# Performance work log

Hardware: AMD Instinct MI355X
Metric: run time of the kernel (lower is better)

The kernel has to match this reference:

```python
import jax, jax.numpy as jnp
import numpy as np

BLOCK = 64


def setup_inputs() -> dict:
    key = jax.random.key(0)
    ks = jax.random.split(key, 8)
    B, S, H = 16, 2048, 768
    E, M, P = 32, 4, 128
    L = 97
    return {
        "task_features": jax.random.normal(ks[0], (B, S, H), dtype=jnp.float32),
        "entity_position_ids": jax.random.randint(ks[1], (B, E, M), 0, S),
        "head_tail_idxs": jax.random.randint(ks[2], (B, P, 2), 0, E),
        "Wh": jax.random.normal(ks[3], (H, H), dtype=jnp.float32) * 0.02,
        "bh": jnp.zeros((H,), dtype=jnp.float32),
        "Wt": jax.random.normal(ks[4], (H, H), dtype=jnp.float32) * 0.02,
        "bt": jnp.zeros((H,), dtype=jnp.float32),
        "Wc": jax.random.normal(ks[5], (H * BLOCK, L), dtype=jnp.float32) * 0.02,
        "bc": jnp.zeros((L,), dtype=jnp.float32),
    }


def reference(task_features, entity_position_ids, head_tail_idxs, Wh, bh, Wt, bt, Wc, bc):
    B, S, H = task_features.shape
    pos = entity_position_ids  # [B, E, M] mention start positions
    # One-hot semantics: indicator[start]=1, so duplicate mention positions within an
    # entity count once. Keep only first occurrence of each position per entity.
    eq = pos[..., :, None] == pos[..., None, :]          # [B, E, M, M]
    dup = jnp.any(jnp.tril(eq, -1), axis=-1)             # equal to an earlier mention
    w = (~dup).astype(task_features.dtype)               # [B, E, M]
    # Gather mention-start features and pool (sum) per entity: [B, E, H]
    feats = task_features[jnp.arange(B)[:, None, None], pos]  # [B, E, M, H]
    ent = jnp.einsum('bemh,bem->beh', feats, w)
    # Select subject/object entity representations per pair
    bi = jnp.arange(B)[:, None]
    subj = ent[bi, head_tail_idxs[..., 0]].reshape(-1, H)  # [B*P, H]
    obj = ent[bi, head_tail_idxs[..., 1]].reshape(-1, H)
    z_s = jnp.tanh(subj @ Wh + bh)
    z_o = jnp.tanh(obj @ Wt + bt)
    N = z_s.shape[0]
    b1 = z_s.reshape(N, H // BLOCK, BLOCK)
    b2 = z_o.reshape(N, H // BLOCK, BLOCK)
    # Block-bilinear: per-block outer product -> [N, H*BLOCK]
    bl = (b1[..., :, None] * b2[..., None, :]).reshape(N, H * BLOCK)
    logits = bl @ Wc + bc  # [N, 97]
    return logits
```

## Files before the change

kernel.cpp:

```cpp
#include <hip/hip_runtime.h>
#include <hip/hip_bf16.h>

typedef __bf16 bf16_t;
typedef bf16_t bf16x8 __attribute__((ext_vector_type(8)));
typedef float  f32x4  __attribute__((ext_vector_type(4)));

#define B_    16
#define S_    2048
#define H_    768
#define E_    32
#define M_    4
#define P_    128
#define L_    97
#define NPAIR 2048
#define RSPLIT 48

#define OFF_WHT  0u
#define OFF_WTT  (OFF_WHT + 768u*768u*2u)
#define OFF_WCG  (OFF_WTT + 768u*768u*2u)
#define OFF_ENT  (OFF_WCG + 768u*14336u)
#define OFF_ZS   (OFF_ENT + 512u*768u*2u)
#define OFF_ZO   (OFF_ZS  + 512u*768u*2u)
#define OFF_PART (OFF_ZO  + 512u*768u*2u)

typedef __attribute__((address_space(1))) const unsigned gu32;
typedef __attribute__((address_space(3))) unsigned lu32;

static __device__ __forceinline__ float bf_lo(unsigned u) { return __builtin_bit_cast(float, u << 16); }
static __device__ __forceinline__ float bf_hi(unsigned u) { return __builtin_bit_cast(float, u & 0xffff0000u); }
static __device__ __forceinline__ unsigned short bf_bits(float f) {
    return __builtin_bit_cast(unsigned short, (bf16_t)f);
}

__global__ __launch_bounds__(256) void k_transpose_w(const float* __restrict__ Wh,
                                                     const float* __restrict__ Wt,
                                                     bf16_t* __restrict__ whT,
                                                     bf16_t* __restrict__ wtT) {
    __shared__ float tile[32][33];
    const float* W = blockIdx.z ? Wt : Wh;
    bf16_t* WT = blockIdx.z ? wtT : whT;
    int k0 = blockIdx.x * 32, c0 = blockIdx.y * 32;
    int tx = threadIdx.x & 31, ty = threadIdx.x >> 5;
    for (int r = 0; r < 4; r++) {
        int ky = ty + r * 8;
        tile[ky][tx] = W[(k0 + ky) * H_ + c0 + tx];
    }
    __syncthreads();
    for (int r = 0; r < 4; r++) {
        int cy = ty + r * 8;
        WT[(c0 + cy) * H_ + (k0 + tx)] = (bf16_t)tile[tx][cy];
    }
}

__global__ __launch_bounds__(256) void k_build_wcg(const float* __restrict__ Wc,
                                                   unsigned* __restrict__ wcg) {
    int I = blockIdx.x;
    unsigned base_dw = (unsigned)I * 3584u;
    for (int r = 0; r < 14; r++) {
        int d  = threadIdx.x + 256 * r;
        int l  = d >> 5;
        int gp = (d >> 2) & 7;
        int k  = d & 3;
        int gl = gp ^ (l & 7);
        int j  = (gl * 4 + k) * 2;
        int p  = I * 64 + j;
        float v0 = (l < L_) ? Wc[(size_t)p * L_ + l]       : 0.f;
        float v1 = (l < L_) ? Wc[(size_t)(p + 1) * L_ + l] : 0.f;
        unsigned pk = (unsigned)bf_bits(v0) | ((unsigned)bf_bits(v1) << 16);
        wcg[base_dw + d] = pk;
    }
}

__global__ __launch_bounds__(256) void k_ent(const float* __restrict__ tf,
                                             const int* __restrict__ pos,
                                             bf16_t* __restrict__ ent) {
    int be = blockIdx.x;
    int b  = be >> 5;
    int p0 = pos[be*4+0], p1 = pos[be*4+1], p2 = pos[be*4+2], p3 = pos[be*4+3];
    bool w1 = (p1 != p0);
    bool w2 = (p2 != p0) && (p2 != p1);
    bool w3 = (p3 != p0) && (p3 != p1) && (p3 != p2);
    const float* base = tf + (size_t)b * S_ * H_;
    for (int qq = 0; qq < 3; qq++) {
        int h = threadIdx.x + qq * 256;
        float s = base[(size_t)p0 * H_ + h];
        if (w1) s += base[(size_t)p1 * H_ + h];
        if (w2) s += base[(size_t)p2 * H_ + h];
        if (w3) s += base[(size_t)p3 * H_ + h];
        ent[(size_t)be * H_ + h] = (bf16_t)s;
    }
}

__global__ __launch_bounds__(256) void k_gemm_z(const bf16_t* __restrict__ ent,
                                                const bf16_t* __restrict__ whT,
                                                const bf16_t* __restrict__ wtT,
                                                const float* __restrict__ bh,
                                                const float* __restrict__ bt,
                                                bf16_t* __restrict__ zs,
                                                bf16_t* __restrict__ zo) {
    const bf16_t* WT  = blockIdx.z ? wtT : whT;
    const float* bias = blockIdx.z ? bt  : bh;
    bf16_t* outp      = blockIdx.z ? zo  : zs;
    int w = threadIdx.x >> 6, lane = threadIdx.x & 63;
    int ml = lane & 15, q = lane >> 4;
    int m0 = blockIdx.x * 64 + w * 16;
    int c0 = blockIdx.y * 64;
    f32x4 zero4 = {0.f, 0.f, 0.f, 0.f};
    f32x4 acc[4] = {zero4, zero4, zero4, zero4};
    const bf16_t* aptr = ent + (size_t)(m0 + ml) * H_ + q * 8;
    for (int kk = 0; kk < 24; kk++) {
        bf16x8 a = *reinterpret_cast<const bf16x8*>(aptr + kk * 32);
        for (int lt = 0; lt < 4; lt++) {
            const bf16_t* bp = WT + (size_t)(c0 + lt * 16 + ml) * H_ + kk * 32 + q * 8;
            bf16x8 bfr = *reinterpret_cast<const bf16x8*>(bp);
            acc[lt] = __builtin_amdgcn_mfma_f32_16x16x32_bf16(a, bfr, acc[lt], 0, 0, 0);
        }
    }
    for (int lt = 0; lt < 4; lt++)
        for (int r = 0; r < 4; r++) {
            int row = q * 4 + r;
            int col = c0 + lt * 16 + ml;
            float v = tanhf(acc[lt][r] + bias[col]);
            outp[(size_t)(m0 + row) * H_ + col] = (bf16_t)v;
        }
}

__global__ __launch_bounds__(256) void k_bilinear(const bf16_t* __restrict__ zs,
                                                  const bf16_t* __restrict__ zo,
                                                  const unsigned* __restrict__ wcg,
                                                  const int* __restrict__ ht,
                                                  float* __restrict__ pout) {
    __shared__ __align__(16) unsigned wc_lds[2][112 * 32];
    __shared__ unsigned short zs_lds[16 * 256];
    int nb = blockIdx.x;
    int c  = blockIdx.y;
    int I0 = c * 16;
    int kblk = I0 >> 6;
    int i0   = I0 & 63;
    int t = threadIdx.x;
    int w = t >> 6, lane = t & 63, ml = lane & 15, q = lane >> 4;
    int nbase = nb * 256;

    {
        int n  = nbase + t;
        int es = (n >> 7) * E_ + ht[n * 2 + 0];
        const unsigned short* src =
            reinterpret_cast<const unsigned short*>(zs) + (size_t)es * H_ + kblk * 64 + i0;
        uint4 u0 = *reinterpret_cast<const uint4*>(src);
        uint4 u1 = *reinterpret_cast<const uint4*>(src + 8);
        unsigned vals[8] = {u0.x, u0.y, u0.z, u0.w, u1.x, u1.y, u1.z, u1.w};
        for (int d = 0; d < 8; d++) {
            zs_lds[(2 * d) * 256 + t]     = (unsigned short)(vals[d] & 0xffffu);
            zs_lds[(2 * d + 1) * 256 + t] = (unsigned short)(vals[d] >> 16);
        }
    }

    bf16x8 zoA[4][2];
    for (int nt = 0; nt < 4; nt++) {
        int n  = nbase + w * 64 + nt * 16 + ml;
        int eo = (n >> 7) * E_ + ht[n * 2 + 1];
        const bf16_t* src = zo + (size_t)eo * H_ + kblk * 64;
        zoA[nt][0] = *reinterpret_cast<const bf16x8*>(src + 0 * 32 + q * 8);
        zoA[nt][1] = *reinterpret_cast<const bf16x8*>(src + 1 * 32 + q * 8);
    }

    f32x4 zero4 = {0.f, 0.f, 0.f, 0.f};
    f32x4 acc[4][7];
    for (int nt = 0; nt < 4; nt++)
        for (int lt = 0; lt < 7; lt++) acc[nt][lt] = zero4;

    const unsigned* gsrc = wcg + (size_t)I0 * 3584u;

    for (int pp = w; pp < 14; pp += 4)
        __builtin_amdgcn_global_load_lds((gu32*)(gsrc + pp * 256 + lane * 4),
                                         (lu32*)&wc_lds[0][pp * 256], 16, 0, 0);
    __syncthreads();

    int sw = ml & 7;
    for (int ii = 0; ii < 16; ii++) {
        int pb = ii & 1;
        if (ii < 15) {
            const unsigned* g2 = gsrc + (size_t)(ii + 1) * 3584u;
            for (int pp = w; pp < 14; pp += 4)
                __builtin_amdgcn_global_load_lds((gu32*)(g2 + pp * 256 + lane * 4),
                                                 (lu32*)&wc_lds[1 - pb][pp * 256], 16, 0, 0);
        }

        float zsv[4][4];
        for (int nt = 0; nt < 4; nt++) {
            const unsigned* zp = reinterpret_cast<const unsigned*>(
                &zs_lds[ii * 256 + w * 64 + nt * 16 + q * 4]);
            unsigned z0 = zp[0], z1 = zp[1];
            zsv[nt][0] = bf_lo(z0); zsv[nt][1] = bf_hi(z0);
            zsv[nt][2] = bf_lo(z1); zsv[nt][3] = bf_hi(z1);
        }

        const unsigned short* wch = reinterpret_cast<const unsigned short*>(wc_lds[pb]);
        for (int lt = 0; lt < 7; lt++) {
            int l = lt * 16 + ml;
            bf16x8 b0 = *reinterpret_cast<const bf16x8*>(wch + l * 64 + ((q ^ sw) * 8));
            bf16x8 b1 = *reinterpret_cast<const bf16x8*>(wch + l * 64 + (((4 + q) ^ sw) * 8));
            for (int nt = 0; nt < 4; nt++) {
                f32x4 dres = __builtin_amdgcn_mfma_f32_16x16x32_bf16(zoA[nt][0], b0, zero4, 0, 0, 0);
                dres = __builtin_amdgcn_mfma_f32_16x16x32_bf16(zoA[nt][1], b1, dres, 0, 0, 0);
                for (int r = 0; r < 4; r++) acc[nt][lt][r] += zsv[nt][r] * dres[r];
            }
        }
        __syncthreads();
    }

    float* po = pout + ((size_t)c * NPAIR + nbase) * 112;
    for (int nt = 0; nt < 4; nt++)
        for (int lt = 0; lt < 7; lt++)
            for (int r = 0; r < 4; r++) {
                int nl = w * 64 + nt * 16 + q * 4 + r;
                po[(size_t)nl * 112 + lt * 16 + ml] = acc[nt][lt][r];
            }
}

__global__ __launch_bounds__(256) void k_reduce(const float* __restrict__ part,
                                                const float* __restrict__ bc,
                                                float* __restrict__ out) {
    int t = blockIdx.x * 256 + threadIdx.x;
    if (t >= NPAIR * L_) return;
    int n = t / L_;
    int l = t - n * L_;
    float s = bc[l];
    const float* p = part + (size_t)n * 112 + l;
    #pragma unroll
    for (int cc = 0; cc < RSPLIT; cc++) s += p[(size_t)cc * NPAIR * 112];
    out[t] = s;
}

extern "C" void kernel_launch(void* const* d_in, const int* in_sizes, int n_in,
                              void* d_out, int out_size, void* d_ws, size_t ws_size,
                              hipStream_t stream) {
    (void)in_sizes; (void)n_in; (void)out_size; (void)ws_size;
    const float* tf  = (const float*)d_in[0];
    const int*   pos = (const int*)d_in[1];
    const int*   ht  = (const int*)d_in[2];
    const float* Wh  = (const float*)d_in[3];
    const float* bh  = (const float*)d_in[4];
    const float* Wt  = (const float*)d_in[5];
    const float* bt  = (const float*)d_in[6];
    const float* Wc  = (const float*)d_in[7];
    const float* bc  = (const float*)d_in[8];
    float* out = (float*)d_out;
    char*  ws  = (char*)d_ws;

    bf16_t*   whT  = (bf16_t*)(ws + OFF_WHT);
    bf16_t*   wtT  = (bf16_t*)(ws + OFF_WTT);
    unsigned* wcg  = (unsigned*)(ws + OFF_WCG);
    bf16_t*   ent  = (bf16_t*)(ws + OFF_ENT);
    bf16_t*   zsp  = (bf16_t*)(ws + OFF_ZS);
    bf16_t*   zop  = (bf16_t*)(ws + OFF_ZO);
    float*    part = (float*)(ws + OFF_PART);

    k_transpose_w<<<dim3(24, 24, 2), 256, 0, stream>>>(Wh, Wt, whT, wtT);
    k_build_wcg  <<<dim3(768), 256, 0, stream>>>(Wc, wcg);
    k_ent        <<<dim3(512), 256, 0, stream>>>(tf, pos, ent);
    k_gemm_z     <<<dim3(8, 12, 2), 256, 0, stream>>>(ent, whT, wtT, bh, bt, zsp, zop);
    k_bilinear   <<<dim3(8, RSPLIT), 256, 0, stream>>>(zsp, zop, wcg, ht, part);
    k_reduce     <<<dim3((NPAIR * L_ + 255) / 256), 256, 0, stream>>>(part, bc, out);
}
```

Measured before the change: 248.2 us.

## Merge prep kernels, widen bilinear blocks to 512 threads, vectorize reduce

Folds the three preprocessing kernels (weight transpose, Wc repacking, entity pooling) into one launch that dispatches on block index, removing two kernel launches. The bilinear kernel now runs 512 threads per block with 8 waves of 32 pairs each instead of 4 waves of 64, halving per-thread accumulators to raise occupancy. The reduction reads float4 partials and writes four labels per thread. The main risk is the extra barrier cost of the larger bilinear blocks and the less even work split inside the merged prep kernel.

```diff
diff --git a/kernel.cpp b/kernel.cpp
--- a/kernel.cpp
+++ b/kernel.cpp
@@ -32,62 +32,65 @@
     return __builtin_bit_cast(unsigned short, (bf16_t)f);
 }
 
-__global__ __launch_bounds__(256) void k_transpose_w(const float* __restrict__ Wh,
-                                                     const float* __restrict__ Wt,
-                                                     bf16_t* __restrict__ whT,
-                                                     bf16_t* __restrict__ wtT) {
-    __shared__ float tile[32][33];
-    const float* W = blockIdx.z ? Wt : Wh;
-    bf16_t* WT = blockIdx.z ? wtT : whT;
-    int k0 = blockIdx.x * 32, c0 = blockIdx.y * 32;
-    int tx = threadIdx.x & 31, ty = threadIdx.x >> 5;
-    for (int r = 0; r < 4; r++) {
-        int ky = ty + r * 8;
-        tile[ky][tx] = W[(k0 + ky) * H_ + c0 + tx];
-    }
-    __syncthreads();
-    for (int r = 0; r < 4; r++) {
-        int cy = ty + r * 8;
-        WT[(c0 + cy) * H_ + (k0 + tx)] = (bf16_t)tile[tx][cy];
-    }
-}
-
-__global__ __launch_bounds__(256) void k_build_wcg(const float* __restrict__ Wc,
-                                                   unsigned* __restrict__ wcg) {
-    int I = blockIdx.x;
-    unsigned base_dw = (unsigned)I * 3584u;
-    for (int r = 0; r < 14; r++) {
-        int d  = threadIdx.x + 256 * r;
-        int l  = d >> 5;
-        int gp = (d >> 2) & 7;
-        int k  = d & 3;
-        int gl = gp ^ (l & 7);
-        int j  = (gl * 4 + k) * 2;
-        int p  = I * 64 + j;
-        float v0 = (l < L_) ? Wc[(size_t)p * L_ + l]       : 0.f;
-        float v1 = (l < L_) ? Wc[(size_t)(p + 1) * L_ + l] : 0.f;
-        unsigned pk = (unsigned)bf_bits(v0) | ((unsigned)bf_bits(v1) << 16);
-        wcg[base_dw + d] = pk;
-    }
-}
-
-__global__ __launch_bounds__(256) void k_ent(const float* __restrict__ tf,
-                                             const int* __restrict__ pos,
-                                             bf16_t* __restrict__ ent) {
-    int be = blockIdx.x;
-    int b  = be >> 5;
-    int p0 = pos[be*4+0], p1 = pos[be*4+1], p2 = pos[be*4+2], p3 = pos[be*4+3];
-    bool w1 = (p1 != p0);
-    bool w2 = (p2 != p0) && (p2 != p1);
-    bool w3 = (p3 != p0) && (p3 != p1) && (p3 != p2);
-    const float* base = tf + (size_t)b * S_ * H_;
-    for (int qq = 0; qq < 3; qq++) {
-        int h = threadIdx.x + qq * 256;
-        float s = base[(size_t)p0 * H_ + h];
-        if (w1) s += base[(size_t)p1 * H_ + h];
-        if (w2) s += base[(size_t)p2 * H_ + h];
-        if (w3) s += base[(size_t)p3 * H_ + h];
-        ent[(size_t)be * H_ + h] = (bf16_t)s;
+__global__ __launch_bounds__(256) void k_prep(const float* __restrict__ Wh,
+                                              const float* __restrict__ Wt,
+                                              const float* __restrict__ Wc,
+                                              const float* __restrict__ tf,
+                                              const int* __restrict__ pos,
+                                              bf16_t* __restrict__ whT,
+                                              bf16_t* __restrict__ wtT,
+                                              unsigned* __restrict__ wcg,
+                                              bf16_t* __restrict__ ent) {
+    int bid = blockIdx.x;
+    if (bid < 1152) {
+        __shared__ float tile[32][33];
+        int z   = bid / 576;
+        int rem = bid - z * 576;
+        const float* W = z ? Wt : Wh;
+        bf16_t* WT = z ? wtT : whT;
+        int k0 = (rem % 24) * 32, c0 = (rem / 24) * 32;
+        int tx = threadIdx.x & 31, ty = threadIdx.x >> 5;
+        for (int r = 0; r < 4; r++) {
+            int ky = ty + r * 8;
+            tile[ky][tx] = W[(k0 + ky) * H_ + c0 + tx];
+        }
+        __syncthreads();
+        for (int r = 0; r < 4; r++) {
+            int cy = ty + r * 8;
+            WT[(c0 + cy) * H_ + (k0 + tx)] = (bf16_t)tile[tx][cy];
+        }
+    } else if (bid < 1920) {
+        int I = bid - 1152;
+        unsigned base_dw = (unsigned)I * 3584u;
+        for (int r = 0; r < 14; r++) {
+            int d  = threadIdx.x + 256 * r;
+            int l  = d >> 5;
+            int gp = (d >> 2) & 7;
+            int k  = d & 3;
+            int gl = gp ^ (l & 7);
+            int j  = (gl * 4 + k) * 2;
+            int p  = I * 64 + j;
+            float v0 = (l < L_) ? Wc[(size_t)p * L_ + l]       : 0.f;
+            float v1 = (l < L_) ? Wc[(size_t)(p + 1) * L_ + l] : 0.f;
+            unsigned pk = (unsigned)bf_bits(v0) | ((unsigned)bf_bits(v1) << 16);
+            wcg[base_dw + d] = pk;
+        }
+    } else {
+        int be = bid - 1920;
+        int b  = be >> 5;
+        int p0 = pos[be*4+0], p1 = pos[be*4+1], p2 = pos[be*4+2], p3 = pos[be*4+3];
+        bool w1 = (p1 != p0);
+        bool w2 = (p2 != p0) && (p2 != p1);
+        bool w3 = (p3 != p0) && (p3 != p1) && (p3 != p2);
+        const float* base = tf + (size_t)b * S_ * H_;
+        for (int qq = 0; qq < 3; qq++) {
+            int h = threadIdx.x + qq * 256;
+            float s = base[(size_t)p0 * H_ + h];
+            if (w1) s += base[(size_t)p1 * H_ + h];
+            if (w2) s += base[(size_t)p2 * H_ + h];
+            if (w3) s += base[(size_t)p3 * H_ + h];
+            ent[(size_t)be * H_ + h] = (bf16_t)s;
+        }
     }
 }
 
@@ -125,11 +128,11 @@
         }
 }
 
-__global__ __launch_bounds__(256) void k_bilinear(const bf16_t* __restrict__ zs,
-                                                  const bf16_t* __restrict__ zo,
-                                                  const unsigned* __restrict__ wcg,
-                                                  const int* __restrict__ ht,
-                                                  float* __restrict__ pout) {
+__global__ __launch_bounds__(512, 3) void k_bilinear(const bf16_t* __restrict__ zs,
+                                                     const bf16_t* __restrict__ zo,
+                                                     const unsigned* __restrict__ wcg,
+                                                     const int* __restrict__ ht,
+                                                     float* __restrict__ pout) {
     __shared__ __align__(16) unsigned wc_lds[2][112 * 32];
     __shared__ unsigned short zs_lds[16 * 256];
     int nb = blockIdx.x;
@@ -141,7 +144,7 @@
     int w = t >> 6, lane = t & 63, ml = lane & 15, q = lane >> 4;
     int nbase = nb * 256;
 
-    {
+    if (t < 256) {
         int n  = nbase + t;
         int es = (n >> 7) * E_ + ht[n * 2 + 0];
         const unsigned short* src =
@@ -155,9 +158,9 @@
         }
     }
 
-    bf16x8 zoA[4][2];
-    for (int nt = 0; nt < 4; nt++) {
-        int n  = nbase + w * 64 + nt * 16 + ml;
+    bf16x8 zoA[2][2];
+    for (int nt = 0; nt < 2; nt++) {
+        int n  = nbase + (w * 2 + nt) * 16 + ml;
         int eo = (n >> 7) * E_ + ht[n * 2 + 1];
         const bf16_t* src = zo + (size_t)eo * H_ + kblk * 64;
         zoA[nt][0] = *reinterpret_cast<const bf16x8*>(src + 0 * 32 + q * 8);
@@ -165,13 +168,13 @@
     }
 
     f32x4 zero4 = {0.f, 0.f, 0.f, 0.f};
-    f32x4 acc[4][7];
-    for (int nt = 0; nt < 4; nt++)
+    f32x4 acc[2][7];
+    for (int nt = 0; nt < 2; nt++)
         for (int lt = 0; lt < 7; lt++) acc[nt][lt] = zero4;
 
     const unsigned* gsrc = wcg + (size_t)I0 * 3584u;
 
-    for (int pp = w; pp < 14; pp += 4)
+    for (int pp = w; pp < 14; pp += 8)
         __builtin_amdgcn_global_load_lds((gu32*)(gsrc + pp * 256 + lane * 4),
                                          (lu32*)&wc_lds[0][pp * 256], 16, 0, 0);
     __syncthreads();
@@ -181,15 +184,15 @@
         int pb = ii & 1;
         if (ii < 15) {
             const unsigned* g2 = gsrc + (size_t)(ii + 1) * 3584u;
-            for (int pp = w; pp < 14; pp += 4)
+            for (int pp = w; pp < 14; pp += 8)
                 __builtin_amdgcn_global_load_lds((gu32*)(g2 + pp * 256 + lane * 4),
                                                  (lu32*)&wc_lds[1 - pb][pp * 256], 16, 0, 0);
         }
 
-        float zsv[4][4];
-        for (int nt = 0; nt < 4; nt++) {
+        float zsv[2][4];
+        for (int nt = 0; nt < 2; nt++) {
             const unsigned* zp = reinterpret_cast<const unsigned*>(
-                &zs_lds[ii * 256 + w * 64 + nt * 16 + q * 4]);
+                &zs_lds[ii * 256 + (w * 2 + nt) * 16 + q * 4]);
             unsigned z0 = zp[0], z1 = zp[1];
             zsv[nt][0] = bf_lo(z0); zsv[nt][1] = bf_hi(z0);
             zsv[nt][2] = bf_lo(z1); zsv[nt][3] = bf_hi(z1);
@@ -200,7 +203,7 @@
             int l = lt * 16 + ml;
             bf16x8 b0 = *reinterpret_cast<const bf16x8*>(wch + l * 64 + ((q ^ sw) * 8));
             bf16x8 b1 = *reinterpret_cast<const bf16x8*>(wch + l * 64 + (((4 + q) ^ sw) * 8));
-            for (int nt = 0; nt < 4; nt++) {
+            for (int nt = 0; nt < 2; nt++) {
                 f32x4 dres = __builtin_amdgcn_mfma_f32_16x16x32_bf16(zoA[nt][0], b0, zero4, 0, 0, 0);
                 dres = __builtin_amdgcn_mfma_f32_16x16x32_bf16(zoA[nt][1], b1, dres, 0, 0, 0);
                 for (int r = 0; r < 4; r++) acc[nt][lt][r] += zsv[nt][r] * dres[r];
@@ -210,10 +213,10 @@
     }
 
     float* po = pout + ((size_t)c * NPAIR + nbase) * 112;
-    for (int nt = 0; nt < 4; nt++)
+    for (int nt = 0; nt < 2; nt++)
         for (int lt = 0; lt < 7; lt++)
             for (int r = 0; r < 4; r++) {
-                int nl = w * 64 + nt * 16 + q * 4 + r;
+                int nl = (w * 2 + nt) * 16 + q * 4 + r;
                 po[(size_t)nl * 112 + lt * 16 + ml] = acc[nt][lt][r];
             }
 }
@@ -222,14 +225,21 @@
                                                 const float* __restrict__ bc,
                                                 float* __restrict__ out) {
     int t = blockIdx.x * 256 + threadIdx.x;
-    if (t >= NPAIR * L_) return;
-    int n = t / L_;
-    int l = t - n * L_;
-    float s = bc[l];
-    const float* p = part + (size_t)n * 112 + l;
+    if (t >= NPAIR * 28) return;
+    int n  = t / 28;
+    int l4 = (t - n * 28) * 4;
+    const float* p = part + (size_t)n * 112 + l4;
+    f32x4 s = {0.f, 0.f, 0.f, 0.f};
     #pragma unroll
-    for (int cc = 0; cc < RSPLIT; cc++) s += p[(size_t)cc * NPAIR * 112];
-    out[t] = s;
+    for (int cc = 0; cc < RSPLIT; cc++) {
+        f32x4 v = *reinterpret_cast<const f32x4*>(p + (size_t)cc * NPAIR * 112);
+        s += v;
+    }
+    #pragma unroll
+    for (int e = 0; e < 4; e++) {
+        int l = l4 + e;
+        if (l < L_) out[(size_t)n * L_ + l] = s[e] + bc[l];
+    }
 }
 
 extern "C" void kernel_launch(void* const* d_in, const int* in_sizes, int n_in,
@@ -256,10 +266,8 @@
     bf16_t*   zop  = (bf16_t*)(ws + OFF_ZO);
     float*    part = (float*)(ws + OFF_PART);
 
-    k_transpose_w<<<dim3(24, 24, 2), 256, 0, stream>>>(Wh, Wt, whT, wtT);
-    k_build_wcg  <<<dim3(768), 256, 0, stream>>>(Wc, wcg);
-    k_ent        <<<dim3(512), 256, 0, stream>>>(tf, pos, ent);
-    k_gemm_z     <<<dim3(8, 12, 2), 256, 0, stream>>>(ent, whT, wtT, bh, bt, zsp, zop);
-    k_bilinear   <<<dim3(8, RSPLIT), 256, 0, stream>>>(zsp, zop, wcg, ht, part);
-    k_reduce     <<<dim3((NPAIR * L_ + 255) / 256), 256, 0, stream>>>(part, bc, out);
-}
+    k_prep    <<<dim3(2432), 256, 0, stream>>>(Wh, Wt, Wc, tf, pos, whT, wtT, wcg, ent);
+    k_gemm_z  <<<dim3(8, 12, 2), 256, 0, stream>>>(ent, whT, wtT, bh, bt, zsp, zop);
+    k_bilinear<<<dim3(8, RSPLIT), 512, 0, stream>>>(zsp, zop, wcg, ht, part);
+    k_reduce  <<<dim3((NPAIR * 28 + 255) / 256), 256, 0, stream>>>(part, bc, out);
+}
```

Result: faster. 230.5 us (-7.1%).
